# Performance work log

Hardware: AMD Instinct MI355X
Metric: run time of the kernel (lower is better)

Reference implementation:

```python
import jax, jax.numpy as jnp
import numpy as np

ALPHA = 0.2  # LeakyReLU negative slope
NEG_INF = -1.0e9

def gat_layer(h, adj_mask, W, a, concat):
    # h: [B,N,Fin], W: [Fout,Fin] (torch Linear layout), a: [2*Fout]
    Wh = jnp.einsum('bni,oi->bno', h, W)  # [B,N,Fout]
    F_out = W.shape[0]
    # a([Wh_i, Wh_j]) = Wh_i . a[:F] + Wh_j . a[F:]  (avoids O(N^2*2F) concat, same math)
    s_src = Wh @ a[:F_out]  # [B,N]
    s_dst = Wh @ a[F_out:]  # [B,N]
    e = jax.nn.leaky_relu(s_src[:, :, None] + s_dst[:, None, :], ALPHA)  # [B,N,N]
    e = jnp.where(adj_mask, e, NEG_INF)
    att = jax.nn.softmax(e, axis=-1)  # dropout is identity in eval mode
    h_prime = jnp.einsum('bij,bjf->bif', att, Wh)
    return jax.nn.elu(h_prime) if concat else h_prime

def setup_inputs() -> dict:
    key = jax.random.key(0)
    ks = jax.random.split(key, 8)
    B, N = 4, 2048
    IN, HID, OUT, H = 64, 64, 32, 4
    x = jax.random.normal(ks[0], (B, N, IN), dtype=jnp.float32)
    adj = jax.random.randint(ks[1], (B, N, N), 0, 2, dtype=jnp.int32)

    def xavier(k, shape):
        fan_out, fan_in = shape[0], shape[1]
        lim = float(np.sqrt(6.0 / (fan_in + fan_out)))
        return jax.random.uniform(k, shape, jnp.float32, -lim, lim)

    W1 = jnp.stack([xavier(jax.random.fold_in(ks[2], i), (HID, IN)) for i in range(H)])      # [H,64,64]
    a1 = jnp.stack([xavier(jax.random.fold_in(ks[3], i), (1, 2 * HID))[0] for i in range(H)])  # [H,128]
    W2 = xavier(ks[4], (OUT, H * HID))  # [32,256]
    a2 = xavier(ks[5], (1, 2 * OUT))[0]  # [64]
    return {"x": x, "adj": adj, "W1": W1, "a1": a1, "W2": W2, "a2": a2}

def reference(x, adj, W1, a1, W2, a2):
    mask = adj > 0
    # layer 1: num_heads concat heads with ELU
    heads = [gat_layer(x, mask, W1[k], a1[k], True) for k in range(W1.shape[0])]
    h = jnp.concatenate(heads, axis=-1)  # [B,N,H*HID]
    # output layer: single head, no ELU
    return gat_layer(h, mask, W2, a2, False)
```

## Files before the change

### kernel.cpp

```cpp
#include <hip/hip_runtime.h>
#include <hip/hip_bf16.h>
#include <cstdint>

#define NN 2048
#define NH 4
#define NW 64

typedef __attribute__((ext_vector_type(8))) short bf16x8;
typedef __attribute__((ext_vector_type(4))) float f32x4;
typedef __attribute__((ext_vector_type(4))) int i32x4;
typedef __attribute__((ext_vector_type(4))) unsigned short u16x4;

__device__ __forceinline__ float lrelu(float s) { return s > 0.f ? s : 0.2f * s; }

__device__ __forceinline__ unsigned pk2(float lo, float hi) {
  __hip_bfloat162 h2 = __float22bfloat162_rn(make_float2(lo, hi));
  union { __hip_bfloat162 h; unsigned u; } c; c.h = h2; return c.u;
}
__device__ __forceinline__ short f2bf1(float f) {
  __hip_bfloat16 h = __float2bfloat16(f);
  union { __hip_bfloat16 h; unsigned short u; } c; c.h = h; return (short)c.u;
}
__device__ __forceinline__ bf16x8 cvt8(f32x4 v0, f32x4 v1) {
  union { unsigned u[4]; bf16x8 v; } r;
  r.u[0] = pk2(v0[0], v0[1]); r.u[1] = pk2(v0[2], v0[3]);
  r.u[2] = pk2(v1[0], v1[1]); r.u[3] = pk2(v1[2], v1[3]);
  return r.v;
}


__global__ __launch_bounds__(256) void kA(
    const int* __restrict__ adj, unsigned* __restrict__ mb,
    const float* __restrict__ x, const float* __restrict__ W1,
    const float* __restrict__ a1, unsigned short* __restrict__ wht1,
    float* __restrict__ ssrc1, float* __restrict__ G1g, float* __restrict__ G2g) {
  if (blockIdx.x >= 512) {
    int pb = blockIdx.x - 512;
    int t = threadIdx.x;
    const i32x4* ap = (const i32x4*)adj + ((size_t)pb * 256 + t) * 4;
    i32x4 v0 = __builtin_nontemporal_load(ap + 0);
    i32x4 v1 = __builtin_nontemporal_load(ap + 1);
    i32x4 v2 = __builtin_nontemporal_load(ap + 2);
    i32x4 v3 = __builtin_nontemporal_load(ap + 3);
    unsigned msk = 0;
    msk |= (unsigned)(v0[0] != 0) | ((unsigned)(v0[1] != 0) << 1) |
           ((unsigned)(v0[2] != 0) << 2) | ((unsigned)(v0[3] != 0) << 3);
    msk |= ((unsigned)(v1[0] != 0) << 4) | ((unsigned)(v1[1] != 0) << 5) |
           ((unsigned)(v1[2] != 0) << 6) | ((unsigned)(v1[3] != 0) << 7);
    msk |= ((unsigned)(v2[0] != 0) << 8) | ((unsigned)(v2[1] != 0) << 9) |
           ((unsigned)(v2[2] != 0) << 10) | ((unsigned)(v2[3] != 0) << 11);
    msk |= ((unsigned)(v3[0] != 0) << 12) | ((unsigned)(v3[1] != 0) << 13) |
           ((unsigned)(v3[2] != 0) << 14) | ((unsigned)(v3[3] != 0) << 15);
    unsigned other = __shfl_xor(msk, 1);
    if (!(t & 1)) mb[pb * 128 + (t >> 1)] = msk | (other << 16);
    return;
  }
  int blk = blockIdx.x;
  int rowg = blk * 16;
  int b = rowg >> 11, rloc = rowg & (NN - 1);
  int tid = threadIdx.x, lane = tid & 63, h = tid >> 6;
  int cl = lane & 15, g = lane >> 4;

  const float* xr = x + (size_t)(rowg + cl) * 64 + 8 * g;
  bf16x8 af[2];
#pragma unroll
  for (int ks = 0; ks < 2; ++ks)
    af[ks] = cvt8(*(const f32x4*)(xr + ks * 32), *(const f32x4*)(xr + ks * 32 + 4));

  f32x4 zero = {0.f, 0.f, 0.f, 0.f};
  f32x4 acc[4] = {zero, zero, zero, zero};
#pragma unroll
  for (int ft = 0; ft < 4; ++ft) {
    const float* wr = W1 + (size_t)(h * 64 + ft * 16 + cl) * 64 + 8 * g;
#pragma unroll
    for (int ks = 0; ks < 2; ++ks) {
      bf16x8 bfr = cvt8(*(const f32x4*)(wr + ks * 32), *(const f32x4*)(wr + ks * 32 + 4));
      acc[ft] = __builtin_amdgcn_mfma_f32_16x16x32_bf16(af[ks], bfr, acc[ft], 0, 0, 0);
    }
  }
  unsigned short* bhb = wht1 + (size_t)(b * NH + h) * 64 * NN;
  int kb = rloc >> 5;
  int gd = ((rloc >> 3) & 2) + (g >> 1);
  int e0 = 4 * (g & 1);
  float ps[4] = {0.f, 0.f, 0.f, 0.f}, pd[4] = {0.f, 0.f, 0.f, 0.f};
#pragma unroll
  for (int ft = 0; ft < 4; ++ft) {
    float as = a1[h * 128 + ft * 16 + cl];
    float ad = a1[h * 128 + 64 + ft * 16 + cl];
    u16x4 w4;
#pragma unroll
    for (int r = 0; r < 4; ++r) {
      float v = acc[ft][r];
      w4[r] = (unsigned short)f2bf1(v);
      ps[r] += v * as; pd[r] += v * ad;
    }
    *(u16x4*)(bhb + (size_t)(kb * 4 + ft) * 512 + cl * 8 + gd * 128 + e0) = w4;
  }
#pragma unroll
  for (int r = 0; r < 4; ++r) {
    float s = ps[r], d = pd[r];
    s += __shfl_xor(s, 1); s += __shfl_xor(s, 2); s += __shfl_xor(s, 4); s += __shfl_xor(s, 8);
    d += __shfl_xor(d, 1); d += __shfl_xor(d, 2); d += __shfl_xor(d, 4); d += __shfl_xor(d, 8);
    if (cl == 0) {
      int idx = (b * NH + h) * NN + rloc + 4 * g + r;
      ssrc1[idx] = s;
      G1g[idx] = __expf(d);
      G2g[idx] = __expf(0.2f * d);
    }
  }
}

__global__ __launch_bounds__(512) void k2_attn1(
    const unsigned short* __restrict__ wht1, const float* __restrict__ ssrc1,
    const float* __restrict__ G1g, const float* __restrict__ G2g,
    const unsigned* __restrict__ mb, float* __restrict__ hout) {
  __shared__ __align__(16) char smem[33280];
  __shared__ float swmax[8];
  unsigned (*sdm)[65] = (unsigned(*)[65])smem;
  float* sG1 = (float*)(smem + 16640);
  float* sG2 = (float*)(smem + 16640 + 8192);
  float (*cmb)[16][68] = (float(*)[16][68])smem;
  float (*sden)[16] = (float(*)[16])(smem + 17408);

  int bid = blockIdx.x;
  int bh = bid & 15, tile = bid >> 4;
  int b = bh >> 2, h = bh & 3;
  int rowblk = tile << 6;
  int t = threadIdx.x, lane = t & 63, w = t >> 6;
  int wloc = w & 3, jh = w >> 2;
  int cl = lane & 15, g = lane >> 4, g8 = g * 8;

  {
    int row = t >> 3, c = (t & 7) * 8;
    const unsigned* mrow = mb + (size_t)(b * NN + rowblk + row) * NW + c;
    uint4 v0 = *(const uint4*)(mrow);
    uint4 v1 = *(const uint4*)(mrow + 4);
    sdm[row][c + 0] = v0.x; sdm[row][c + 1] = v0.y;
    sdm[row][c + 2] = v0.z; sdm[row][c + 3] = v0.w;
    sdm[row][c + 4] = v1.x; sdm[row][c + 5] = v1.y;
    sdm[row][c + 6] = v1.z; sdm[row][c + 7] = v1.w;
  }
  {
    const f32x4* g1p = (const f32x4*)(G1g + (size_t)(b * NH + h) * NN);
    const f32x4* g2p = (const f32x4*)(G2g + (size_t)(b * NH + h) * NN);
    f32x4 gv = g1p[t];
    ((f32x4*)sG1)[t] = gv;
    ((f32x4*)sG2)[t] = g2p[t];
    float gmx = fmaxf(fmaxf(gv[0], gv[1]), fmaxf(gv[2], gv[3]));
    gmx = fmaxf(gmx, __shfl_xor(gmx, 1));  gmx = fmaxf(gmx, __shfl_xor(gmx, 2));
    gmx = fmaxf(gmx, __shfl_xor(gmx, 4));  gmx = fmaxf(gmx, __shfl_xor(gmx, 8));
    gmx = fmaxf(gmx, __shfl_xor(gmx, 16)); gmx = fmaxf(gmx, __shfl_xor(gmx, 32));
    if (lane == 0) swmax[w] = gmx;
  }
  int rowW = rowblk + wloc * 16;
  float s = ssrc1[(size_t)(b * NH + h) * NN + rowW + cl];
  __syncthreads();
  float mxv = fmaxf(fmaxf(fmaxf(swmax[0], swmax[1]), fmaxf(swmax[2], swmax[3])),
                    fmaxf(fmaxf(swmax[4], swmax[5]), fmaxf(swmax[6], swmax[7])));
  float logMx = __logf(mxv);
  float m = lrelu(s + logMx);
  float F1 = __expf(s - m), F2 = __expf(0.2f * s - m);

  short onev = (cl == 0) ? (short)0x3F80 : (short)0;
  bf16x8 ones = {onev, onev, onev, onev, onev, onev, onev, onev};
  f32x4 zero = {0.f, 0.f, 0.f, 0.f};
  f32x4 acc[4] = {zero, zero, zero, zero};
  f32x4 acc1 = zero;
  const unsigned short* fbase = wht1 + (size_t)(b * NH + h) * 64 * NN + lane * 8;
  int rloc = wloc * 16 + cl;
  int kb0 = jh * 32;

  bf16x8 curf[4], nxtf[4];
#pragma unroll
  for (int ft = 0; ft < 4; ++ft)
    curf[ft] = *(const bf16x8*)(fbase + (size_t)(kb0 * 4 + ft) * 512);

  for (int i = 0; i < 32; ++i) {
    int kb = kb0 + i;
    if (i < 31) {
#pragma unroll
      for (int ft = 0; ft < 4; ++ft)
        nxtf[ft] = *(const bf16x8*)(fbase + (size_t)((kb + 1) * 4 + ft) * 512);
    }
    unsigned by = (sdm[rloc][kb] >> g8) & 0xFFu;
    int j0 = kb * 32 + g8;
    f32x4 g1a = *(const f32x4*)(sG1 + j0);
    f32x4 g1b = *(const f32x4*)(sG1 + j0 + 4);
    f32x4 g2a = *(const f32x4*)(sG2 + j0);
    f32x4 g2b = *(const f32x4*)(sG2 + j0 + 4);
    float wv[8];
#pragma unroll
    for (int e = 0; e < 8; ++e) {
      float g1 = (e < 4) ? g1a[e] : g1b[e - 4];
      float g2 = (e < 4) ? g2a[e] : g2b[e - 4];
      float v = fmaxf(F1 * g1, F2 * g2);
      wv[e] = ((by >> e) & 1u) ? v : 0.f;
    }
    union { unsigned u[4]; bf16x8 v; } pa;
    pa.u[0] = pk2(wv[0], wv[1]); pa.u[1] = pk2(wv[2], wv[3]);
    pa.u[2] = pk2(wv[4], wv[5]); pa.u[3] = pk2(wv[6], wv[7]);
#pragma unroll
    for (int ft = 0; ft < 4; ++ft)
      acc[ft] = __builtin_amdgcn_mfma_f32_16x16x32_bf16(pa.v, curf[ft], acc[ft], 0, 0, 0);
    acc1 = __builtin_amdgcn_mfma_f32_16x16x32_bf16(pa.v, ones, acc1, 0, 0, 0);
#pragma unroll
    for (int ft = 0; ft < 4; ++ft) curf[ft] = nxtf[ft];
  }
  __syncthreads();
  if (jh == 1) {
#pragma unroll
    for (int ft = 0; ft < 4; ++ft)
#pragma unroll
      for (int r = 0; r < 4; ++r)
        cmb[wloc][4 * g + r][ft * 16 + cl] = acc[ft][r];
    if (cl == 0) {
#pragma unroll
      for (int r = 0; r < 4; ++r) sden[wloc][4 * g + r] = acc1[r];
    }
  }
  __syncthreads();
  if (jh == 0) {
#pragma unroll
    for (int r = 0; r < 4; ++r) {
      int rowm = 4 * g + r;
      float dself = __shfl(acc1[r], lane & 48);
      float inv = 1.f / (dself + sden[wloc][rowm]);
      float* dst = hout + (size_t)(b * NN + rowW + rowm) * 256 + h * 64;
#pragma unroll
      for (int ft = 0; ft < 4; ++ft) {
        float v = (acc[ft][r] + cmb[wloc][rowm][ft * 16 + cl]) * inv;
        v = v > 0.f ? v : (__expf(v) - 1.f);
        dst[ft * 16 + cl] = v;
      }
    }
  }
}

__global__ __launch_bounds__(256) void k3_proj2(
    const float* __restrict__ hin, const float* __restrict__ W2,
    const float* __restrict__ a2, unsigned short* __restrict__ wh2t,
    float* __restrict__ ssrc2, float* __restrict__ G1o, float* __restrict__ G2o) {
  __shared__ float cmb[4][16][33];
  int blk = blockIdx.x;
  int b = blk >> 7, rowbase = (blk & 127) << 4;
  int t = threadIdx.x, lane = t & 63, w = t >> 6;
  int cl = lane & 15, g = lane >> 4;
  int k0 = w * 64;

  const float* hr = hin + (size_t)(b * NN + rowbase + cl) * 256 + k0 + 8 * g;
  bf16x8 af[2];
#pragma unroll
  for (int ks = 0; ks < 2; ++ks)
    af[ks] = cvt8(*(const f32x4*)(hr + ks * 32), *(const f32x4*)(hr + ks * 32 + 4));

  f32x4 zero = {0.f, 0.f, 0.f, 0.f};
  f32x4 acc[2] = {zero, zero};
#pragma unroll
  for (int ft = 0; ft < 2; ++ft) {
    const float* wr = W2 + (size_t)(ft * 16 + cl) * 256 + k0 + 8 * g;
#pragma unroll
    for (int ks = 0; ks < 2; ++ks) {
      bf16x8 bfr = cvt8(*(const f32x4*)(wr + ks * 32), *(const f32x4*)(wr + ks * 32 + 4));
      acc[ft] = __builtin_amdgcn_mfma_f32_16x16x32_bf16(af[ks], bfr, acc[ft], 0, 0, 0);
    }
  }
#pragma unroll
  for (int ft = 0; ft < 2; ++ft)
#pragma unroll
    for (int r = 0; r < 4; ++r)
      cmb[w][4 * g + r][ft * 16 + cl] = acc[ft][r];
  __syncthreads();

  int row = t >> 4, c0 = t & 15;
  float v0 = cmb[0][row][c0] + cmb[1][row][c0] + cmb[2][row][c0] + cmb[3][row][c0];
  float v1 = cmb[0][row][c0 + 16] + cmb[1][row][c0 + 16] + cmb[2][row][c0 + 16] + cmb[3][row][c0 + 16];
  float ps = v0 * a2[c0] + v1 * a2[c0 + 16];
  float pd = v0 * a2[32 + c0] + v1 * a2[32 + c0 + 16];
  ps += __shfl_xor(ps, 1); ps += __shfl_xor(ps, 2); ps += __shfl_xor(ps, 4); ps += __shfl_xor(ps, 8);
  pd += __shfl_xor(pd, 1); pd += __shfl_xor(pd, 2); pd += __shfl_xor(pd, 4); pd += __shfl_xor(pd, 8);
  if (c0 == 0) {
    int idx = b * NN + rowbase + row;
    ssrc2[idx] = ps;
    G1o[idx] = __expf(pd);
    G2o[idx] = __expf(0.2f * pd);
  }
  cmb[0][row][c0] = v0;
  cmb[0][row][c0 + 16] = v1;
  __syncthreads();
  int col = t >> 3, rg = t & 7;
  unsigned pk = pk2(cmb[0][2 * rg][col], cmb[0][2 * rg + 1][col]);
  int kb2 = rowbase >> 5;
  int gd = ((rowbase >> 3) & 2) + (rg >> 2);
  size_t off = (size_t)(kb2 * 2 + (col >> 4)) * 512 + (col & 15) * 8 + gd * 128 + 2 * (rg & 3);
  *(unsigned*)(wh2t + (size_t)b * 32 * NN + off) = pk;
}

__global__ __launch_bounds__(512) void k4_attn2(
    const unsigned short* __restrict__ wh2t, const float* __restrict__ ssrc2,
    const float* __restrict__ G1o, const float* __restrict__ G2o,
    const unsigned* __restrict__ mb, float* __restrict__ outp) {
  __shared__ unsigned sdm[16][65];
  __shared__ __align__(16) float sG1[NN], sG2[NN];
  __shared__ float pacc[16 * 33];
  __shared__ float pden[16];
  __shared__ float swmax[8];
  int blk = blockIdx.x;
  int b = blk >> 7, rowbase = (blk & 127) << 4;
  int t = threadIdx.x, lane = t & 63, w = t >> 6;
  int cl = lane & 15, g = lane >> 4, g8 = g * 8;
  {
    int row = t >> 5, c = (t & 31) * 2;
    uint2 v = *(const uint2*)(mb + (size_t)(b * NN + rowbase + row) * NW + c);
    sdm[row][c + 0] = v.x; sdm[row][c + 1] = v.y;
  }
  {
    const f32x4* g1p = (const f32x4*)(G1o + (size_t)b * NN);
    const f32x4* g2p = (const f32x4*)(G2o + (size_t)b * NN);
    f32x4 gv = g1p[t];
    ((f32x4*)sG1)[t] = gv;
    ((f32x4*)sG2)[t] = g2p[t];
    float gmx = fmaxf(fmaxf(gv[0], gv[1]), fmaxf(gv[2], gv[3]));
    gmx = fmaxf(gmx, __shfl_xor(gmx, 1));  gmx = fmaxf(gmx, __shfl_xor(gmx, 2));
    gmx = fmaxf(gmx, __shfl_xor(gmx, 4));  gmx = fmaxf(gmx, __shfl_xor(gmx, 8));
    gmx = fmaxf(gmx, __shfl_xor(gmx, 16)); gmx = fmaxf(gmx, __shfl_xor(gmx, 32));
    if (lane == 0) swmax[w] = gmx;
  }
  for (int i = t; i < 16 * 33; i += 512) pacc[i] = 0.f;
  if (t < 16) pden[t] = 0.f;
  float s = ssrc2[b * NN + rowbase + cl];
  __syncthreads();
  float mxv = fmaxf(fmaxf(fmaxf(swmax[0], swmax[1]), fmaxf(swmax[2], swmax[3])),
                    fmaxf(fmaxf(swmax[4], swmax[5]), fmaxf(swmax[6], swmax[7])));
  float logMx = __logf(mxv);
  float m = lrelu(s + logMx);
  float F1 = __expf(s - m), F2 = __expf(0.2f * s - m);

  short onev = (cl == 0) ? (short)0x3F80 : (short)0;
  bf16x8 ones = {onev, onev, onev, onev, onev, onev, onev, onev};
  f32x4 zero = {0.f, 0.f, 0.f, 0.f};
  f32x4 acc[2] = {zero, zero};
  f32x4 acc1 = zero;
  const unsigned short* fbase = wh2t + (size_t)b * 32 * NN + lane * 8;
  int kb0 = w * 8;

  bf16x8 curf[2], nxtf[2];
#pragma unroll
  for (int ft = 0; ft < 2; ++ft)
    curf[ft] = *(const bf16x8*)(fbase + (size_t)(kb0 * 2 + ft) * 512);

  for (int i = 0; i < 8; ++i) {
    int kb = kb0 + i;
    if (i < 7) {
#pragma unroll
      for (int ft = 0; ft < 2; ++ft)
        nxtf[ft] = *(const bf16x8*)(fbase + (size_t)((kb + 1) * 2 + ft) * 512);
    }
    unsigned by = (sdm[cl][kb] >> g8) & 0xFFu;
    int j0 = kb * 32 + g8;
    f32x4 g1a = *(const f32x4*)(sG1 + j0);
    f32x4 g1b = *(const f32x4*)(sG1 + j0 + 4);
    f32x4 g2a = *(const f32x4*)(sG2 + j0);
    f32x4 g2b = *(const f32x4*)(sG2 + j0 + 4);
    float wv[8];
#pragma unroll
    for (int e = 0; e < 8; ++e) {
      float g1 = (e < 4) ? g1a[e] : g1b[e - 4];
      float g2 = (e < 4) ? g2a[e] : g2b[e - 4];
      float v = fmaxf(F1 * g1, F2 * g2);
      wv[e] = ((by >> e) & 1u) ? v : 0.f;
    }
    union { unsigned u[4]; bf16x8 v; } pa;
    pa.u[0] = pk2(wv[0], wv[1]); pa.u[1] = pk2(wv[2], wv[3]);
    pa.u[2] = pk2(wv[4], wv[5]); pa.u[3] = pk2(wv[6], wv[7]);
#pragma unroll
    for (int ft = 0; ft < 2; ++ft)
      acc[ft] = __builtin_amdgcn_mfma_f32_16x16x32_bf16(pa.v, curf[ft], acc[ft], 0, 0, 0);
    acc1 = __builtin_amdgcn_mfma_f32_16x16x32_bf16(pa.v, ones, acc1, 0, 0, 0);
#pragma unroll
    for (int ft = 0; ft < 2; ++ft) curf[ft] = nxtf[ft];
  }
#pragma unroll
  for (int ft = 0; ft < 2; ++ft)
#pragma unroll
    for (int r = 0; r < 4; ++r)
      atomicAdd(&pacc[(4 * g + r) * 33 + ft * 16 + cl], acc[ft][r]);
  if (cl == 0) {
#pragma unroll
    for (int r = 0; r < 4; ++r) atomicAdd(&pden[4 * g + r], acc1[r]);
  }
  __syncthreads();
  {
    int row = t >> 5, f = t & 31;
    outp[(size_t)(b * NN + rowbase + row) * 32 + f] = pacc[row * 33 + f] / pden[row];
  }
}

extern "C" void kernel_launch(void* const* d_in, const int* in_sizes, int n_in,
                              void* d_out, int out_size, void* d_ws, size_t ws_size,
                              hipStream_t stream) {
  (void)in_sizes; (void)n_in; (void)out_size; (void)ws_size;
  const float* x   = (const float*)d_in[0];
  const int*   adj = (const int*)d_in[1];
  const float* W1  = (const float*)d_in[2];
  const float* a1  = (const float*)d_in[3];
  const float* W2  = (const float*)d_in[4];
  const float* a2  = (const float*)d_in[5];
  float* outp = (float*)d_out;
  char* ws = (char*)d_ws;

  unsigned*       mbits = (unsigned*)(ws);
  unsigned short* wht1  = (unsigned short*)(ws + (size_t)(2u << 20));
  float*          ssrc1 = (float*)(ws + (size_t)(6u << 20));
  float*          G1g   = (float*)(ws + (size_t)(6u << 20) + (128u << 10));
  float*          G2g   = (float*)(ws + (size_t)(6u << 20) + (256u << 10));
  float*          hbuf  = (float*)(ws + (size_t)(6u << 20) + (512u << 10));
  unsigned short* wh2t  = (unsigned short*)(ws + (size_t)(14u << 20) + (512u << 10));
  float*          ssrc2 = (float*)(ws + (size_t)(15u << 20));
  float*          G1o   = (float*)(ws + (size_t)(15u << 20) + (32u << 10));
  float*          G2o   = (float*)(ws + (size_t)(15u << 20) + (64u << 10));

  kA      <<<4608, 256, 0, stream>>>(adj, mbits, x, W1, a1, wht1, ssrc1, G1g, G2g);
  k2_attn1<<<512,  512, 0, stream>>>(wht1, ssrc1, G1g, G2g, mbits, hbuf);
  k3_proj2<<<512,  256, 0, stream>>>(hbuf, W2, a2, wh2t, ssrc2, G1o, G2o);
  k4_attn2<<<512,  512, 0, stream>>>(wh2t, ssrc2, G1o, G2o, mbits, outp);
}
```

Before: 168.3 us.

## Store layer-1 output as bf16, widen mask packing, retile second attention kernel

```diff
diff --git a/kernel.cpp b/kernel.cpp
--- a/kernel.cpp
+++ b/kernel.cpp
@@ -17,9 +17,9 @@
   __hip_bfloat162 h2 = __float22bfloat162_rn(make_float2(lo, hi));
   union { __hip_bfloat162 h; unsigned u; } c; c.h = h2; return c.u;
 }
-__device__ __forceinline__ short f2bf1(float f) {
+__device__ __forceinline__ unsigned short f2bf1(float f) {
   __hip_bfloat16 h = __float2bfloat16(f);
-  union { __hip_bfloat16 h; unsigned short u; } c; c.h = h; return (short)c.u;
+  union { __hip_bfloat16 h; unsigned short u; } c; c.h = h; return c.u;
 }
 __device__ __forceinline__ bf16x8 cvt8(f32x4 v0, f32x4 v1) {
   union { unsigned u[4]; bf16x8 v; } r;
@@ -35,24 +35,29 @@
     const float* __restrict__ a1, unsigned short* __restrict__ wht1,
     float* __restrict__ ssrc1, float* __restrict__ G1g, float* __restrict__ G2g) {
   if (blockIdx.x >= 512) {
-    int pb = blockIdx.x - 512;
-    int t = threadIdx.x;
-    const i32x4* ap = (const i32x4*)adj + ((size_t)pb * 256 + t) * 4;
+    size_t gid = (size_t)(blockIdx.x - 512) * 256 + threadIdx.x;
+    const i32x4* ap = (const i32x4*)adj + gid * 8;
     i32x4 v0 = __builtin_nontemporal_load(ap + 0);
     i32x4 v1 = __builtin_nontemporal_load(ap + 1);
     i32x4 v2 = __builtin_nontemporal_load(ap + 2);
     i32x4 v3 = __builtin_nontemporal_load(ap + 3);
-    unsigned msk = 0;
-    msk |= (unsigned)(v0[0] != 0) | ((unsigned)(v0[1] != 0) << 1) |
-           ((unsigned)(v0[2] != 0) << 2) | ((unsigned)(v0[3] != 0) << 3);
-    msk |= ((unsigned)(v1[0] != 0) << 4) | ((unsigned)(v1[1] != 0) << 5) |
-           ((unsigned)(v1[2] != 0) << 6) | ((unsigned)(v1[3] != 0) << 7);
-    msk |= ((unsigned)(v2[0] != 0) << 8) | ((unsigned)(v2[1] != 0) << 9) |
-           ((unsigned)(v2[2] != 0) << 10) | ((unsigned)(v2[3] != 0) << 11);
-    msk |= ((unsigned)(v3[0] != 0) << 12) | ((unsigned)(v3[1] != 0) << 13) |
-           ((unsigned)(v3[2] != 0) << 14) | ((unsigned)(v3[3] != 0) << 15);
-    unsigned other = __shfl_xor(msk, 1);
-    if (!(t & 1)) mb[pb * 128 + (t >> 1)] = msk | (other << 16);
+    i32x4 v4 = __builtin_nontemporal_load(ap + 4);
+    i32x4 v5 = __builtin_nontemporal_load(ap + 5);
+    i32x4 v6 = __builtin_nontemporal_load(ap + 6);
+    i32x4 v7 = __builtin_nontemporal_load(ap + 7);
+    unsigned word = 0;
+#pragma unroll
+    for (int j = 0; j < 4; ++j) {
+      word |= ((unsigned)(v0[j] != 0)) << (0 + j);
+      word |= ((unsigned)(v1[j] != 0)) << (4 + j);
+      word |= ((unsigned)(v2[j] != 0)) << (8 + j);
+      word |= ((unsigned)(v3[j] != 0)) << (12 + j);
+      word |= ((unsigned)(v4[j] != 0)) << (16 + j);
+      word |= ((unsigned)(v5[j] != 0)) << (20 + j);
+      word |= ((unsigned)(v6[j] != 0)) << (24 + j);
+      word |= ((unsigned)(v7[j] != 0)) << (28 + j);
+    }
+    mb[gid] = word;
     return;
   }
   int blk = blockIdx.x;
@@ -91,7 +96,7 @@
 #pragma unroll
     for (int r = 0; r < 4; ++r) {
       float v = acc[ft][r];
-      w4[r] = (unsigned short)f2bf1(v);
+      w4[r] = f2bf1(v);
       ps[r] += v * as; pd[r] += v * ad;
     }
     *(u16x4*)(bhb + (size_t)(kb * 4 + ft) * 512 + cl * 8 + gd * 128 + e0) = w4;
@@ -113,7 +118,7 @@
 __global__ __launch_bounds__(512) void k2_attn1(
     const unsigned short* __restrict__ wht1, const float* __restrict__ ssrc1,
     const float* __restrict__ G1g, const float* __restrict__ G2g,
-    const unsigned* __restrict__ mb, float* __restrict__ hout) {
+    const unsigned* __restrict__ mb, unsigned short* __restrict__ hout) {
   __shared__ __align__(16) char smem[33280];
   __shared__ float swmax[8];
   unsigned (*sdm)[65] = (unsigned(*)[65])smem;
@@ -225,19 +230,19 @@
       int rowm = 4 * g + r;
       float dself = __shfl(acc1[r], lane & 48);
       float inv = 1.f / (dself + sden[wloc][rowm]);
-      float* dst = hout + (size_t)(b * NN + rowW + rowm) * 256 + h * 64;
+      unsigned short* dst = hout + (size_t)(b * NN + rowW + rowm) * 256 + h * 64;
 #pragma unroll
       for (int ft = 0; ft < 4; ++ft) {
         float v = (acc[ft][r] + cmb[wloc][rowm][ft * 16 + cl]) * inv;
         v = v > 0.f ? v : (__expf(v) - 1.f);
-        dst[ft * 16 + cl] = v;
+        dst[ft * 16 + cl] = f2bf1(v);
       }
     }
   }
 }
 
 __global__ __launch_bounds__(256) void k3_proj2(
-    const float* __restrict__ hin, const float* __restrict__ W2,
+    const unsigned short* __restrict__ hin, const float* __restrict__ W2,
     const float* __restrict__ a2, unsigned short* __restrict__ wh2t,
     float* __restrict__ ssrc2, float* __restrict__ G1o, float* __restrict__ G2o) {
   __shared__ float cmb[4][16][33];
@@ -247,11 +252,11 @@
   int cl = lane & 15, g = lane >> 4;
   int k0 = w * 64;
 
-  const float* hr = hin + (size_t)(b * NN + rowbase + cl) * 256 + k0 + 8 * g;
+  const unsigned short* hr = hin + (size_t)(b * NN + rowbase + cl) * 256 + k0 + 8 * g;
   bf16x8 af[2];
 #pragma unroll
   for (int ks = 0; ks < 2; ++ks)
-    af[ks] = cvt8(*(const f32x4*)(hr + ks * 32), *(const f32x4*)(hr + ks * 32 + 4));
+    af[ks] = *(const bf16x8*)(hr + ks * 32);
 
   f32x4 zero = {0.f, 0.f, 0.f, 0.f};
   f32x4 acc[2] = {zero, zero};
@@ -299,35 +304,39 @@
     const unsigned short* __restrict__ wh2t, const float* __restrict__ ssrc2,
     const float* __restrict__ G1o, const float* __restrict__ G2o,
     const unsigned* __restrict__ mb, float* __restrict__ outp) {
-  __shared__ unsigned sdm[16][65];
-  __shared__ __align__(16) float sG1[NN], sG2[NN];
-  __shared__ float pacc[16 * 33];
-  __shared__ float pden[16];
+  __shared__ __align__(16) char smem[24704];
   __shared__ float swmax[8];
-  int blk = blockIdx.x;
-  int b = blk >> 7, rowbase = (blk & 127) << 4;
+  unsigned (*sdm)[65] = (unsigned(*)[65])smem;
+  float* sG1 = (float*)(smem + 8320);
+  float* sG2 = (float*)(smem + 8320 + 8192);
+  float (*cmb)[2][16][36] = (float(*)[2][16][36])smem;
+  float (*sden)[2][16] = (float(*)[2][16])(smem + 13824);
+
+  int bid = blockIdx.x;
+  int b = bid & 3, tile = bid >> 2;
+  int rowblk = tile << 5;
   int t = threadIdx.x, lane = t & 63, w = t >> 6;
+  int wloc = w & 1, jh = w >> 1;
   int cl = lane & 15, g = lane >> 4, g8 = g * 8;
+
   {
-    int row = t >> 5, c = (t & 31) * 2;
-    uint2 v = *(const uint2*)(mb + (size_t)(b * NN + rowbase + row) * NW + c);
+    int row = t >> 4, c = (t & 15) * 4;
+    uint4 v = *(const uint4*)(mb + (size_t)(b * NN + rowblk + row) * NW + c);
     sdm[row][c + 0] = v.x; sdm[row][c + 1] = v.y;
+    sdm[row][c + 2] = v.z; sdm[row][c + 3] = v.w;
   }
   {
-    const f32x4* g1p = (const f32x4*)(G1o + (size_t)b * NN);
-    const f32x4* g2p = (const f32x4*)(G2o + (size_t)b * NN);
-    f32x4 gv = g1p[t];
+    f32x4 gv = ((const f32x4*)(G1o + (size_t)b * NN))[t];
     ((f32x4*)sG1)[t] = gv;
-    ((f32x4*)sG2)[t] = g2p[t];
+    ((f32x4*)sG2)[t] = ((const f32x4*)(G2o + (size_t)b * NN))[t];
     float gmx = fmaxf(fmaxf(gv[0], gv[1]), fmaxf(gv[2], gv[3]));
     gmx = fmaxf(gmx, __shfl_xor(gmx, 1));  gmx = fmaxf(gmx, __shfl_xor(gmx, 2));
     gmx = fmaxf(gmx, __shfl_xor(gmx, 4));  gmx = fmaxf(gmx, __shfl_xor(gmx, 8));
     gmx = fmaxf(gmx, __shfl_xor(gmx, 16)); gmx = fmaxf(gmx, __shfl_xor(gmx, 32));
     if (lane == 0) swmax[w] = gmx;
   }
-  for (int i = t; i < 16 * 33; i += 512) pacc[i] = 0.f;
-  if (t < 16) pden[t] = 0.f;
-  float s = ssrc2[b * NN + rowbase + cl];
+  int rowW = rowblk + wloc * 16;
+  float s = ssrc2[b * NN + rowW + cl];
   __syncthreads();
   float mxv = fmaxf(fmaxf(fmaxf(swmax[0], swmax[1]), fmaxf(swmax[2], swmax[3])),
                     fmaxf(fmaxf(swmax[4], swmax[5]), fmaxf(swmax[6], swmax[7])));
@@ -341,21 +350,22 @@
   f32x4 acc[2] = {zero, zero};
   f32x4 acc1 = zero;
   const unsigned short* fbase = wh2t + (size_t)b * 32 * NN + lane * 8;
-  int kb0 = w * 8;
+  int rloc = wloc * 16 + cl;
+  int kb0 = jh * 16;
 
   bf16x8 curf[2], nxtf[2];
 #pragma unroll
   for (int ft = 0; ft < 2; ++ft)
     curf[ft] = *(const bf16x8*)(fbase + (size_t)(kb0 * 2 + ft) * 512);
 
-  for (int i = 0; i < 8; ++i) {
+  for (int i = 0; i < 16; ++i) {
     int kb = kb0 + i;
-    if (i < 7) {
+    if (i < 15) {
 #pragma unroll
       for (int ft = 0; ft < 2; ++ft)
         nxtf[ft] = *(const bf16x8*)(fbase + (size_t)((kb + 1) * 2 + ft) * 512);
     }
-    unsigned by = (sdm[cl][kb] >> g8) & 0xFFu;
+    unsigned by = (sdm[rloc][kb] >> g8) & 0xFFu;
     int j0 = kb * 32 + g8;
     f32x4 g1a = *(const f32x4*)(sG1 + j0);
     f32x4 g1b = *(const f32x4*)(sG1 + j0 + 4);
@@ -379,19 +389,34 @@
 #pragma unroll
     for (int ft = 0; ft < 2; ++ft) curf[ft] = nxtf[ft];
   }
-#pragma unroll
-  for (int ft = 0; ft < 2; ++ft)
-#pragma unroll
-    for (int r = 0; r < 4; ++r)
-      atomicAdd(&pacc[(4 * g + r) * 33 + ft * 16 + cl], acc[ft][r]);
-  if (cl == 0) {
-#pragma unroll
-    for (int r = 0; r < 4; ++r) atomicAdd(&pden[4 * g + r], acc1[r]);
-  }
-  __syncthreads();
-  {
-    int row = t >> 5, f = t & 31;
-    outp[(size_t)(b * NN + rowbase + row) * 32 + f] = pacc[row * 33 + f] / pden[row];
+  __syncthreads();
+  if (jh > 0) {
+#pragma unroll
+    for (int ft = 0; ft < 2; ++ft)
+#pragma unroll
+      for (int r = 0; r < 4; ++r)
+        cmb[jh - 1][wloc][4 * g + r][ft * 16 + cl] = acc[ft][r];
+    if (cl == 0) {
+#pragma unroll
+      for (int r = 0; r < 4; ++r) sden[jh - 1][wloc][4 * g + r] = acc1[r];
+    }
+  }
+  __syncthreads();
+  if (jh == 0) {
+#pragma unroll
+    for (int r = 0; r < 4; ++r) {
+      int rowm = 4 * g + r;
+      float dself = __shfl(acc1[r], lane & 48);
+      float den = dself + sden[0][wloc][rowm] + sden[1][wloc][rowm] + sden[2][wloc][rowm];
+      float inv = 1.f / den;
+      float* dst = outp + (size_t)(b * NN + rowW + rowm) * 32;
+#pragma unroll
+      for (int ft = 0; ft < 2; ++ft) {
+        float v = acc[ft][r] + cmb[0][wloc][rowm][ft * 16 + cl] +
+                  cmb[1][wloc][rowm][ft * 16 + cl] + cmb[2][wloc][rowm][ft * 16 + cl];
+        dst[ft * 16 + cl] = v * inv;
+      }
+    }
   }
 }
 
@@ -413,14 +438,14 @@
   float*          ssrc1 = (float*)(ws + (size_t)(6u << 20));
   float*          G1g   = (float*)(ws + (size_t)(6u << 20) + (128u << 10));
   float*          G2g   = (float*)(ws + (size_t)(6u << 20) + (256u << 10));
-  float*          hbuf  = (float*)(ws + (size_t)(6u << 20) + (512u << 10));
+  unsigned short* hbuf  = (unsigned short*)(ws + (size_t)(6u << 20) + (512u << 10));
   unsigned short* wh2t  = (unsigned short*)(ws + (size_t)(14u << 20) + (512u << 10));
   float*          ssrc2 = (float*)(ws + (size_t)(15u << 20));
   float*          G1o   = (float*)(ws + (size_t)(15u << 20) + (32u << 10));
   float*          G2o   = (float*)(ws + (size_t)(15u << 20) + (64u << 10));
 
-  kA      <<<4608, 256, 0, stream>>>(adj, mbits, x, W1, a1, wht1, ssrc1, G1g, G2g);
+  kA      <<<2560, 256, 0, stream>>>(adj, mbits, x, W1, a1, wht1, ssrc1, G1g, G2g);
   k2_attn1<<<512,  512, 0, stream>>>(wht1, ssrc1, G1g, G2g, mbits, hbuf);
   k3_proj2<<<512,  256, 0, stream>>>(hbuf, W2, a2, wh2t, ssrc2, G1o, G2o);
-  k4_attn2<<<512,  512, 0, stream>>>(wh2t, ssrc2, G1o, G2o, mbits, outp);
-}
+  k4_attn2<<<256,  512, 0, stream>>>(wh2t, ssrc2, G1o, G2o, mbits, outp);
+}
```

Measured after the change: 165.9 us. Within noise of the previous version (-1.5%).
